# Kernel optimization log

Hardware: AMD Instinct MI355X
Metric: run time of the kernel (lower is better)

## Reference

```python
import jax, jax.numpy as jnp
import numpy as np

N_NODES = 100000


def gcn_conv(x, edge_index, W, b):
    # PyG GCNConv: add self-loops, symmetric norm, then scatter-aggregate.
    n = x.shape[0]
    x = x @ W  # [N, out]
    src = jnp.concatenate([edge_index[0], jnp.arange(n)])  # self-loops
    dst = jnp.concatenate([edge_index[1], jnp.arange(n)])
    ones = jnp.ones(src.shape[0], dtype=x.dtype)
    deg = jax.ops.segment_sum(ones, dst, num_segments=n)  # in-degree incl. self-loops
    dis = jnp.where(deg > 0, jax.lax.rsqrt(deg), 0.0)
    norm = dis[src] * dis[dst]  # [E+N]
    msg = x[src] * norm[:, None]  # gather + scale
    out = jax.ops.segment_sum(msg, dst, num_segments=n)
    return out + b


def setup_inputs() -> dict:
    key = jax.random.key(0)
    ks = jax.random.split(key, 8)
    in_dim, h1, h2, out_dim, E = 128, 128, 64, 10, 1600000
    glorot = lambda k, fi, fo: jax.random.normal(k, (fi, fo), jnp.float32) * np.sqrt(2.0 / (fi + fo))
    return {
        "x": jax.random.normal(ks[0], (N_NODES, in_dim), jnp.float32),
        "edge_index": jax.random.randint(ks[1], (2, E), 0, N_NODES, jnp.int64),
        "W1": glorot(ks[2], in_dim, h1),
        "b1": jnp.zeros((h1,), jnp.float32),
        "W2": glorot(ks[3], h1, h2),
        "b2": jnp.zeros((h2,), jnp.float32),
        "Wf": glorot(ks[4], h2, out_dim),
        "bf": jnp.zeros((out_dim,), jnp.float32),
    }


def reference(x, edge_index, W1, b1, W2, b2, Wf, bf):
    h = jax.nn.relu(gcn_conv(x, edge_index, W1, b1))
    h = jax.nn.relu(gcn_conv(h, edge_index, W2, b2))
    logits = h @ Wf + bf
    return jax.nn.softmax(logits, axis=1)
```

## Files before the change

### kernel.cpp

```cpp
#include <hip/hip_runtime.h>
#include <math.h>

#define NN 100000
#define D_IN 128
#define D_H1 128
#define D_H2 64
#define D_O 10
#define NB 256
#define BDIV 391
#define ECH 4096
#define PCAP 7168
#define S_SEG 16
#define SEGW 6250

static const size_t OFF_G1     = 0;
static const size_t OFF_G2     = 25600000;
static const size_t OFF_W1T    = 40000000;
static const size_t OFF_W2T    = 40100000;
static const size_t OFF_PART   = 76800000;
static const size_t OFF_COL    = 90000000;
static const size_t OFF_DIS    = 98000000;
static const size_t OFF_RP     = 98500000;
static const size_t OFF_RE     = 99000000;
static const size_t OFF_CUR    = 99500000;

typedef __attribute__((ext_vector_type(8))) short short8;
typedef __attribute__((ext_vector_type(4))) float floatx4;

__device__ inline unsigned int pack_bf2(float a, float b) {
  unsigned int ua = __float_as_uint(a);
  ua += 0x7fffu + ((ua >> 16) & 1u);
  unsigned int ub = __float_as_uint(b);
  ub += 0x7fffu + ((ub >> 16) & 1u);
  return (ua >> 16) | (ub & 0xffff0000u);
}
__device__ inline unsigned short bf16u(float a) {
  unsigned int ua = __float_as_uint(a);
  ua += 0x7fffu + ((ua >> 16) & 1u);
  return (unsigned short)(ua >> 16);
}
__device__ inline float bflo(unsigned int u) { return __uint_as_float(u << 16); }
__device__ inline float bfhi(unsigned int u) { return __uint_as_float(u & 0xffff0000u); }
__device__ inline short8 as_short8(uint4 u) {
  union { uint4 u4; short8 s8; } c; c.u4 = u; return c.s8;
}
__device__ inline void acc_u4(float* acc, uint4 u) {
  acc[0] += bflo(u.x); acc[1] += bfhi(u.x);
  acc[2] += bflo(u.y); acc[3] += bfhi(u.y);
  acc[4] += bflo(u.z); acc[5] += bfhi(u.z);
  acc[6] += bflo(u.w); acc[7] += bfhi(u.w);
}
__device__ inline void acc_u4s(float* acc, uint4 u, float sc) {
  acc[0] = fmaf(sc, bflo(u.x), acc[0]);
  acc[1] = fmaf(sc, bfhi(u.x), acc[1]);
  acc[2] = fmaf(sc, bflo(u.y), acc[2]);
  acc[3] = fmaf(sc, bfhi(u.y), acc[3]);
  acc[4] = fmaf(sc, bflo(u.z), acc[4]);
  acc[5] = fmaf(sc, bfhi(u.z), acc[5]);
  acc[6] = fmaf(sc, bflo(u.w), acc[6]);
  acc[7] = fmaf(sc, bfhi(u.w), acc[7]);
}

__global__ __launch_bounds__(256) void scatter_pack_kernel(
    const int* __restrict__ src, const int* __restrict__ dst,
    int* __restrict__ cursor, unsigned int* __restrict__ part,
    int E, int nchunk,
    const float* __restrict__ W1, const float* __restrict__ W2,
    unsigned short* __restrict__ w1t, unsigned short* __restrict__ w2t) {
  const int tid = threadIdx.x;
  const int bid = blockIdx.x;
  if (bid >= nchunk) {
    int pb = bid - nchunk;
    if (pb < 64) {
      int o = pb * 256 + tid;
      int nn = o >> 7, k = o & 127;
      w1t[o] = bf16u(W1[(size_t)k * D_H1 + nn]);
    } else {
      int o = (pb - 64) * 256 + tid;
      int nn = o >> 7, k = o & 127;
      w2t[o] = bf16u(W2[(size_t)k * D_H2 + nn]);
    }
    return;
  }
  __shared__ int dloc[ECH];
  __shared__ int cnt[NB];
  __shared__ int rbase[NB];
  __shared__ int rnk[NB];
  cnt[tid] = 0;
  __syncthreads();
  const int e0 = bid * ECH;
#pragma unroll
  for (int i = 0; i < ECH / 256; ++i) {
    int e = e0 + i * 256 + tid;
    int d = (e < E) ? dst[e] : -1;
    dloc[i * 256 + tid] = d;
    if (d >= 0) atomicAdd(&cnt[d / BDIV], 1);
  }
  __syncthreads();
  rbase[tid] = atomicAdd(&cursor[tid], cnt[tid]);
  rnk[tid] = 0;
  __syncthreads();
#pragma unroll
  for (int i = 0; i < ECH / 256; ++i) {
    int e = e0 + i * 256 + tid;
    if (e < E) {
      int d = dloc[i * 256 + tid];
      int s = src[e];
      int b = d / BDIV;
      int r = rbase[b] + atomicAdd(&rnk[b], 1);
      if (r < PCAP)
        part[(size_t)b * PCAP + r] =
            ((unsigned int)(d - b * BDIV) << 17) | (unsigned int)s;
    }
  }
}

#define TOT (BDIV * S_SEG)
__global__ __launch_bounds__(256) void csr_gemm_kernel(
    const unsigned int* __restrict__ part, const int* __restrict__ cursor,
    int* __restrict__ row_ptr, int* __restrict__ row_end,
    float* __restrict__ dis, int* __restrict__ col,
    const float* __restrict__ A_, const unsigned short* __restrict__ w1t,
    unsigned short* __restrict__ g1, int n) {
  __shared__ char smu[53760];
  const int tid = threadIdx.x;

  if (blockIdx.x < NB) {
    int* cnt2 = (int*)smu;
    int* col_s = (int*)(smu + 25056);
    int* wsum = (int*)(smu + 25056 + 28672);
    const int b = blockIdx.x;
    const int lo = b * BDIV;
    const int nn = min(n - lo, BDIV);
    const int ecnt = min(cursor[b], PCAP);
    const int ebase = b * PCAP;
    for (int t = tid; t <= TOT; t += 256) cnt2[t] = 0;
    __syncthreads();
    for (int i0 = 0; i0 < ecnt; i0 += 256) {
      int idx = i0 + tid;
      if (idx < ecnt) {
        unsigned int p = part[(size_t)ebase + idx];
        int s = (int)(p & 0x1FFFFu);
        atomicAdd(&cnt2[(int)(p >> 17) * S_SEG + s / SEGW], 1);
      }
    }
    __syncthreads();
    {
      const int lane = tid & 63;
      const int wv = tid >> 6;
      int carry = 0;
      for (int t0 = 0; t0 < TOT; t0 += 1024) {
        int i0 = t0 + tid * 4;
        int v0 = (i0 + 0 < TOT) ? cnt2[i0 + 0] : 0;
        int v1 = (i0 + 1 < TOT) ? cnt2[i0 + 1] : 0;
        int v2 = (i0 + 2 < TOT) ? cnt2[i0 + 2] : 0;
        int v3 = (i0 + 3 < TOT) ? cnt2[i0 + 3] : 0;
        int ts = v0 + v1 + v2 + v3;
        int incl = ts;
#pragma unroll
        for (int off = 1; off < 64; off <<= 1) {
          int o = __shfl_up(incl, off);
          if (lane >= off) incl += o;
        }
        if (lane == 63) wsum[wv] = incl;
        __syncthreads();
        int wpre = 0;
#pragma unroll
        for (int w = 0; w < 4; ++w)
          if (w < wv) wpre += wsum[w];
        int btot = wsum[0] + wsum[1] + wsum[2] + wsum[3];
        int e = carry + wpre + (incl - ts);
        __syncthreads();
        if (i0 + 0 < TOT) cnt2[i0 + 0] = e;
        if (i0 + 1 < TOT) cnt2[i0 + 1] = e + v0;
        if (i0 + 2 < TOT) cnt2[i0 + 2] = e + v0 + v1;
        if (i0 + 3 < TOT) cnt2[i0 + 3] = e + v0 + v1 + v2;
        carry += btot;
      }
      if (tid == 0) cnt2[TOT] = carry;
    }
    __syncthreads();
    for (int t = tid; t < nn; t += 256) {
      int b0 = cnt2[t * S_SEG];
      int b1 = cnt2[(t + 1) * S_SEG];
      row_ptr[lo + t] = ebase + b0;
      row_end[lo + t] = ebase + b1;
      dis[lo + t] = rsqrtf((float)(b1 - b0) + 1.0f);
    }
    __syncthreads();
    for (int i0 = 0; i0 < ecnt; i0 += 256) {
      int idx = i0 + tid;
      if (idx < ecnt) {
        unsigned int p = part[(size_t)ebase + idx];
        int s = (int)(p & 0x1FFFFu);
        int r = atomicAdd(&cnt2[(int)(p >> 17) * S_SEG + s / SEGW], 1);
        if (r < PCAP) col_s[r] = s;
      }
    }
    __syncthreads();
    for (int idx = tid; idx < ecnt; idx += 256) col[(size_t)ebase + idx] = col_s[idx];
  } else {
    constexpr int K = 128;
    constexpr int NOUT = D_H1;
    constexpr int NT = NOUT / 16;
    constexpr int LDW = K + 8;
    unsigned short* wt = (unsigned short*)smu;
    unsigned short* buf = wt;
    const int gb = blockIdx.x - NB;

    {
      const uint4* wsrc = (const uint4*)w1t;
#pragma unroll
      for (int j = 0; j < NOUT * K / (8 * 256); ++j) {
        int o = tid + j * 256;
        int row = o >> 4;
        int k8 = (o & 15) * 8;
        *(uint4*)(wt + row * LDW + k8) = wsrc[o];
      }
    }

    const int wave = tid >> 6;
    const int lane = tid & 63;
    const int quad = lane >> 4;
    const int cg = lane & 15;
    const int row0w = gb * 64 + wave * 16;

    short8 afr[4];
    {
      int row = row0w + cg;
      if (row > n - 1) row = n - 1;
#pragma unroll
      for (int kb = 0; kb < 4; ++kb) {
        const float* p = A_ + (size_t)row * K + kb * 32 + quad * 8;
        float4 v0 = *(const float4*)(p);
        float4 v1 = *(const float4*)(p + 4);
        uint4 u;
        u.x = pack_bf2(v0.x, v0.y); u.y = pack_bf2(v0.z, v0.w);
        u.z = pack_bf2(v1.x, v1.y); u.w = pack_bf2(v1.z, v1.w);
        afr[kb] = as_short8(u);
      }
    }
    __syncthreads();

    floatx4 acc[NT];
#pragma unroll
    for (int t = 0; t < NT; ++t) acc[t] = (floatx4){0.f, 0.f, 0.f, 0.f};
#pragma unroll
    for (int t = 0; t < NT; ++t) {
      const unsigned short* wrow = wt + (t * 16 + cg) * LDW;
#pragma unroll
      for (int kb = 0; kb < 4; ++kb) {
        short8 bfr = *(const short8*)(wrow + kb * 32 + quad * 8);
        acc[t] = __builtin_amdgcn_mfma_f32_16x16x32_bf16(afr[kb], bfr, acc[t], 0, 0, 0);
      }
    }
    __syncthreads();

    unsigned short* mybuf = buf + wave * 16 * LDW;
#pragma unroll
    for (int t = 0; t < NT; ++t)
#pragma unroll
      for (int r = 0; r < 4; ++r)
        mybuf[(quad * 4 + r) * LDW + t * 16 + cg] = bf16u(acc[t][r]);
    __syncthreads();

    constexpr int CHUNKS = NOUT / 8;
    constexpr int RPI = 64 / CHUNKS;
    int cid = lane % CHUNKS;
    int rs = lane / CHUNKS;
#pragma unroll
    for (int i = 0; i < 16 / RPI; ++i) {
      int r = rs + i * RPI;
      int grow = row0w + r;
      if (grow < n) {
        uint4 u = *(const uint4*)(mybuf + r * LDW + cid * 8);
        *(uint4*)(g1 + (size_t)grow * NOUT + cid * 8) = u;
      }
    }
  }
}

__global__ __launch_bounds__(256) void gather1_gemm2_kernel(
    const unsigned short* __restrict__ g, const int* __restrict__ col,
    const int* __restrict__ row_ptr, const int* __restrict__ row_end,
    const float* __restrict__ dis, const float* __restrict__ b1,
    const unsigned short* __restrict__ w2t,
    unsigned short* __restrict__ g2, int n) {
  constexpr int K = D_H1;
  constexpr int LDW = K + 8;
  constexpr int LDO = 80;
  __shared__ unsigned short wt[D_H2 * LDW];
  __shared__ unsigned short hl[16 * LDW];
  __shared__ unsigned short obuf[16 * LDO];
  const int tid = threadIdx.x;
  const int row0 = blockIdx.x * 16;

  {
    const uint4* wsrc = (const uint4*)w2t;
#pragma unroll
    for (int j = 0; j < 4; ++j) {
      int o = tid + j * 256;
      int row = o >> 4;
      int k8 = (o & 15) * 8;
      *(uint4*)(wt + row * LDW + k8) = wsrc[o];
    }
  }

  {
    const int v = row0 + (tid >> 4);
    const int c = (tid & 15) * 8;
    const int start = row_ptr[v];
    const int end = row_end[v];
    const float dv = dis[v];
    float acc[8];
#pragma unroll
    for (int q = 0; q < 8; ++q) acc[q] = 0.f;
    acc_u4s(acc, *(const uint4*)(g + (size_t)v * K + c), dv);
    int e = start;
    for (; e + 4 <= end; e += 4) {
      int s0 = col[e + 0], s1 = col[e + 1], s2 = col[e + 2], s3 = col[e + 3];
      float q0 = dis[s0], q1 = dis[s1], q2 = dis[s2], q3 = dis[s3];
      uint4 u0 = *(const uint4*)(g + (size_t)s0 * K + c);
      uint4 u1 = *(const uint4*)(g + (size_t)s1 * K + c);
      uint4 u2 = *(const uint4*)(g + (size_t)s2 * K + c);
      uint4 u3 = *(const uint4*)(g + (size_t)s3 * K + c);
      acc_u4s(acc, u0, q0); acc_u4s(acc, u1, q1);
      acc_u4s(acc, u2, q2); acc_u4s(acc, u3, q3);
    }
    for (; e < end; ++e) {
      int s = col[e];
      acc_u4s(acc, *(const uint4*)(g + (size_t)s * K + c), dis[s]);
    }
    float4 bv0 = *(const float4*)(b1 + c);
    float4 bv1 = *(const float4*)(b1 + c + 4);
    float r0 = fmaxf(dv * acc[0] + bv0.x, 0.f);
    float r1 = fmaxf(dv * acc[1] + bv0.y, 0.f);
    float r2 = fmaxf(dv * acc[2] + bv0.z, 0.f);
    float r3 = fmaxf(dv * acc[3] + bv0.w, 0.f);
    float r4 = fmaxf(dv * acc[4] + bv1.x, 0.f);
    float r5 = fmaxf(dv * acc[5] + bv1.y, 0.f);
    float r6 = fmaxf(dv * acc[6] + bv1.z, 0.f);
    float r7 = fmaxf(dv * acc[7] + bv1.w, 0.f);
    uint4 o;
    o.x = pack_bf2(r0, r1);
    o.y = pack_bf2(r2, r3);
    o.z = pack_bf2(r4, r5);
    o.w = pack_bf2(r6, r7);
    *(uint4*)(hl + (tid >> 4) * LDW + c) = o;
  }
  __syncthreads();

  {
    const int wave = tid >> 6;
    const int lane = tid & 63;
    const int quad = lane >> 4;
    const int cg = lane & 15;
    floatx4 acc = (floatx4){0.f, 0.f, 0.f, 0.f};
    const unsigned short* wrow = wt + (wave * 16 + cg) * LDW;
    const unsigned short* arow = hl + cg * LDW;
#pragma unroll
    for (int kb = 0; kb < 4; ++kb) {
      short8 afr = *(const short8*)(arow + kb * 32 + quad * 8);
      short8 bfr = *(const short8*)(wrow + kb * 32 + quad * 8);
      acc = __builtin_amdgcn_mfma_f32_16x16x32_bf16(afr, bfr, acc, 0, 0, 0);
    }
    float4 dv4 = *(const float4*)(dis + row0 + quad * 4);
    float dvs[4] = {dv4.x, dv4.y, dv4.z, dv4.w};
#pragma unroll
    for (int r = 0; r < 4; ++r)
      obuf[(quad * 4 + r) * LDO + wave * 16 + cg] = bf16u(acc[r] * dvs[r]);
  }
  __syncthreads();

  if (tid < 128) {
    int r = tid >> 3;
    int cid = tid & 7;
    uint4 u = *(const uint4*)(obuf + r * LDO + cid * 8);
    *(uint4*)(g2 + (size_t)(row0 + r) * D_H2 + cid * 8) = u;
  }
}

__global__ __launch_bounds__(256) void gather2_final_kernel(
    const unsigned short* __restrict__ g, const int* __restrict__ col,
    const int* __restrict__ row_ptr, const int* __restrict__ row_end,
    const float* __restrict__ dis, const float* __restrict__ b2,
    const float* __restrict__ Wf, const float* __restrict__ bf,
    float* __restrict__ out, int n) {
  constexpr int LDH = 72;
  __shared__ unsigned short ha[32 * LDH];
  __shared__ unsigned short wtf[16 * LDH];
  __shared__ float bfs[D_O];
  __shared__ float ls[32][12];
  const int tid = threadIdx.x;
  if (tid < 128) {
    int nn = tid >> 3;
    int k = (tid & 7) * 8;
    uint4 u;
    if (nn < D_O) {
      u.x = pack_bf2(Wf[(size_t)(k + 0) * D_O + nn], Wf[(size_t)(k + 1) * D_O + nn]);
      u.y = pack_bf2(Wf[(size_t)(k + 2) * D_O + nn], Wf[(size_t)(k + 3) * D_O + nn]);
      u.z = pack_bf2(Wf[(size_t)(k + 4) * D_O + nn], Wf[(size_t)(k + 5) * D_O + nn]);
      u.w = pack_bf2(Wf[(size_t)(k + 6) * D_O + nn], Wf[(size_t)(k + 7) * D_O + nn]);
    } else {
      u = make_uint4(0u, 0u, 0u, 0u);
    }
    *(uint4*)(wtf + nn * LDH + k) = u;
  }
  if (tid < D_O) bfs[tid] = bf[tid];

  const int gid = blockIdx.x * 256 + tid;
  const int v = gid >> 3;
  const int nl = tid >> 3;
  const int c = (tid & 7) * 8;
  if (v < n) {
    int start = row_ptr[v];
    int end = row_end[v];
    float acc[8];
#pragma unroll
    for (int q = 0; q < 8; ++q) acc[q] = 0.f;
    acc_u4(acc, *(const uint4*)(g + (size_t)v * D_H2 + c));
    int e = start;
    for (; e + 4 <= end; e += 4) {
      int s0 = col[e + 0], s1 = col[e + 1], s2 = col[e + 2], s3 = col[e + 3];
      uint4 u0 = *(const uint4*)(g + (size_t)s0 * D_H2 + c);
      uint4 u1 = *(const uint4*)(g + (size_t)s1 * D_H2 + c);
      uint4 u2 = *(const uint4*)(g + (size_t)s2 * D_H2 + c);
      uint4 u3 = *(const uint4*)(g + (size_t)s3 * D_H2 + c);
      acc_u4(acc, u0); acc_u4(acc, u1); acc_u4(acc, u2); acc_u4(acc, u3);
    }
    for (; e < end; ++e) {
      uint4 u = *(const uint4*)(g + (size_t)col[e] * D_H2 + c);
      acc_u4(acc, u);
    }
    float dv = dis[v];
    float4 bv0 = *(const float4*)(b2 + c);
    float4 bv1 = *(const float4*)(b2 + c + 4);
    float r0 = fmaxf(dv * acc[0] + bv0.x, 0.f);
    float r1 = fmaxf(dv * acc[1] + bv0.y, 0.f);
    float r2 = fmaxf(dv * acc[2] + bv0.z, 0.f);
    float r3 = fmaxf(dv * acc[3] + bv0.w, 0.f);
    float r4 = fmaxf(dv * acc[4] + bv1.x, 0.f);
    float r5 = fmaxf(dv * acc[5] + bv1.y, 0.f);
    float r6 = fmaxf(dv * acc[6] + bv1.z, 0.f);
    float r7 = fmaxf(dv * acc[7] + bv1.w, 0.f);
    uint4 o;
    o.x = pack_bf2(r0, r1);
    o.y = pack_bf2(r2, r3);
    o.z = pack_bf2(r4, r5);
    o.w = pack_bf2(r6, r7);
    *(uint4*)(ha + nl * LDH + c) = o;
  }
  __syncthreads();
  {
    const int wave = tid >> 6;
    if (wave < 2) {
      const int lane = tid & 63;
      const int quad = lane >> 4;
      const int cg = lane & 15;
      floatx4 acc = (floatx4){0.f, 0.f, 0.f, 0.f};
      const unsigned short* arow = ha + (wave * 16 + cg) * LDH;
      const unsigned short* wrow = wtf + cg * LDH;
#pragma unroll
      for (int kb = 0; kb < 2; ++kb) {
        short8 afr = *(const short8*)(arow + kb * 32 + quad * 8);
        short8 bfr = *(const short8*)(wrow + kb * 32 + quad * 8);
        acc = __builtin_amdgcn_mfma_f32_16x16x32_bf16(afr, bfr, acc, 0, 0, 0);
      }
      if (cg < D_O) {
        float bb = bfs[cg];
#pragma unroll
        for (int r = 0; r < 4; ++r)
          ls[wave * 16 + quad * 4 + r][cg] = acc[r] + bb;
      }
    }
  }
  __syncthreads();
  if (tid < 32) {
    int v2 = blockIdx.x * 32 + tid;
    if (v2 < n) {
      float m = ls[tid][0];
#pragma unroll
      for (int j = 1; j < D_O; ++j) m = fmaxf(m, ls[tid][j]);
      float s = 0.f;
      float ex[D_O];
#pragma unroll
      for (int j = 0; j < D_O; ++j) { ex[j] = expf(ls[tid][j] - m); s += ex[j]; }
      float inv = 1.0f / s;
#pragma unroll
      for (int j = 0; j < D_O; ++j) ls[tid][j] = ex[j] * inv;
    }
  }
  __syncthreads();
  for (int idx = tid; idx < 32 * D_O; idx += 256) {
    int gidx = blockIdx.x * 32 * D_O + idx;
    if (gidx < n * D_O) out[gidx] = ls[idx / D_O][idx % D_O];
  }
}

extern "C" void kernel_launch(void* const* d_in, const int* in_sizes, int n_in,
                              void* d_out, int out_size, void* d_ws, size_t ws_size,
                              hipStream_t stream) {
  const float* x  = (const float*)d_in[0];
  const int*   ei = (const int*)d_in[1];
  const float* W1 = (const float*)d_in[2];
  const float* b1 = (const float*)d_in[3];
  const float* W2 = (const float*)d_in[4];
  const float* b2 = (const float*)d_in[5];
  const float* Wf = (const float*)d_in[6];
  const float* bf = (const float*)d_in[7];
  float* out = (float*)d_out;

  const int E = in_sizes[1] / 2;
  const int* src = ei;
  const int* dst = ei + E;

  char* ws = (char*)d_ws;
  unsigned short* g1 = (unsigned short*)(ws + OFF_G1);
  unsigned short* g2 = (unsigned short*)(ws + OFF_G2);
  unsigned short* w1t = (unsigned short*)(ws + OFF_W1T);
  unsigned short* w2t = (unsigned short*)(ws + OFF_W2T);
  unsigned int* part = (unsigned int*)(ws + OFF_PART);
  int*   col     = (int*)(ws + OFF_COL);
  float* dis     = (float*)(ws + OFF_DIS);
  int*   row_ptr = (int*)(ws + OFF_RP);
  int*   row_end = (int*)(ws + OFF_RE);
  int*   cursor  = (int*)(ws + OFF_CUR);

  const int nchunk = (E + ECH - 1) / ECH;

  hipMemsetAsync(cursor, 0, NB * sizeof(int), stream);

  scatter_pack_kernel<<<nchunk + 96, 256, 0, stream>>>(
      src, dst, cursor, part, E, nchunk, W1, W2, w1t, w2t);

  csr_gemm_kernel<<<NB + (NN + 63) / 64, 256, 0, stream>>>(
      part, cursor, row_ptr, row_end, dis, col, x, w1t, g1, NN);

  gather1_gemm2_kernel<<<NN / 16, 256, 0, stream>>>(
      g1, col, row_ptr, row_end, dis, b1, w2t, g2, NN);

  gather2_final_kernel<<<(NN + 31) / 32, 256, 0, stream>>>(
      g2, col, row_ptr, row_end, dis, b2, Wf, bf, out, NN);
}
```

Measured before the change: 240.5 us.

## Split feature matrices into column planes and gather each plane separately

Stores the layer features in column-plane layouts (16-wide planes for layer 1, 8-wide for layer 2) so each gather block reads only a narrow slice per node. The intent is better cache locality for random neighbour gathers, since each plane is small enough to stay resident in cache. The source-side normalisation moves into the GEMM epilogue. The CSR build drops the source-segment sort, and the fused kernels are split into separate csr, gemm1, gather1, gemm2, gather2 and head kernels. This adds launches and extra round trips through memory for the intermediate activations, and neighbour lists are no longer sorted by source.

```diff
diff --git a/kernel.cpp b/kernel.cpp
--- a/kernel.cpp
+++ b/kernel.cpp
@@ -10,19 +10,19 @@
 #define BDIV 391
 #define ECH 4096
 #define PCAP 7168
-#define S_SEG 16
-#define SEGW 6250
-
-static const size_t OFF_G1     = 0;
-static const size_t OFF_G2     = 25600000;
-static const size_t OFF_W1T    = 40000000;
-static const size_t OFF_W2T    = 40100000;
-static const size_t OFF_PART   = 76800000;
-static const size_t OFF_COL    = 90000000;
-static const size_t OFF_DIS    = 98000000;
-static const size_t OFF_RP     = 98500000;
-static const size_t OFF_RE     = 99000000;
-static const size_t OFF_CUR    = 99500000;
+
+
+static const size_t OFF_G1  = 0;
+static const size_t OFF_H   = 25600000;
+static const size_t OFF_G2  = 51200000;
+static const size_t OFF_H2  = 64000000;
+static const size_t OFF_W2T = 76800000;
+static const size_t OFF_PART= 76900000;
+static const size_t OFF_COL = 84300000;
+static const size_t OFF_DIS = 91700000;
+static const size_t OFF_RP  = 92200000;
+static const size_t OFF_RE  = 92600000;
+static const size_t OFF_CUR = 93000000;
 
 typedef __attribute__((ext_vector_type(8))) short short8;
 typedef __attribute__((ext_vector_type(4))) float floatx4;
@@ -50,36 +50,18 @@
   acc[4] += bflo(u.z); acc[5] += bfhi(u.z);
   acc[6] += bflo(u.w); acc[7] += bfhi(u.w);
 }
-__device__ inline void acc_u4s(float* acc, uint4 u, float sc) {
-  acc[0] = fmaf(sc, bflo(u.x), acc[0]);
-  acc[1] = fmaf(sc, bfhi(u.x), acc[1]);
-  acc[2] = fmaf(sc, bflo(u.y), acc[2]);
-  acc[3] = fmaf(sc, bfhi(u.y), acc[3]);
-  acc[4] = fmaf(sc, bflo(u.z), acc[4]);
-  acc[5] = fmaf(sc, bfhi(u.z), acc[5]);
-  acc[6] = fmaf(sc, bflo(u.w), acc[6]);
-  acc[7] = fmaf(sc, bfhi(u.w), acc[7]);
-}
 
 __global__ __launch_bounds__(256) void scatter_pack_kernel(
     const int* __restrict__ src, const int* __restrict__ dst,
     int* __restrict__ cursor, unsigned int* __restrict__ part,
     int E, int nchunk,
-    const float* __restrict__ W1, const float* __restrict__ W2,
-    unsigned short* __restrict__ w1t, unsigned short* __restrict__ w2t) {
+    const float* __restrict__ W2, unsigned short* __restrict__ w2t) {
   const int tid = threadIdx.x;
   const int bid = blockIdx.x;
   if (bid >= nchunk) {
-    int pb = bid - nchunk;
-    if (pb < 64) {
-      int o = pb * 256 + tid;
-      int nn = o >> 7, k = o & 127;
-      w1t[o] = bf16u(W1[(size_t)k * D_H1 + nn]);
-    } else {
-      int o = (pb - 64) * 256 + tid;
-      int nn = o >> 7, k = o & 127;
-      w2t[o] = bf16u(W2[(size_t)k * D_H2 + nn]);
-    }
+    int o = (bid - nchunk) * 256 + tid;
+    int nn = o >> 7, k = o & 127;
+    w2t[o] = bf16u(W2[(size_t)k * D_H2 + nn]);
     return;
   }
   __shared__ int dloc[ECH];
@@ -115,185 +97,214 @@
   }
 }
 
-#define TOT (BDIV * S_SEG)
-__global__ __launch_bounds__(256) void csr_gemm_kernel(
+__global__ __launch_bounds__(256) void csr_kernel(
     const unsigned int* __restrict__ part, const int* __restrict__ cursor,
     int* __restrict__ row_ptr, int* __restrict__ row_end,
-    float* __restrict__ dis, int* __restrict__ col,
-    const float* __restrict__ A_, const unsigned short* __restrict__ w1t,
-    unsigned short* __restrict__ g1, int n) {
-  __shared__ char smu[53760];
-  const int tid = threadIdx.x;
-
-  if (blockIdx.x < NB) {
-    int* cnt2 = (int*)smu;
-    int* col_s = (int*)(smu + 25056);
-    int* wsum = (int*)(smu + 25056 + 28672);
-    const int b = blockIdx.x;
-    const int lo = b * BDIV;
-    const int nn = min(n - lo, BDIV);
-    const int ecnt = min(cursor[b], PCAP);
-    const int ebase = b * PCAP;
-    for (int t = tid; t <= TOT; t += 256) cnt2[t] = 0;
+    float* __restrict__ dis, int* __restrict__ col, int n) {
+  __shared__ int sm[256];
+  __shared__ int ldeg[BDIV + 1];
+  __shared__ int lofs[BDIV + 1];
+  __shared__ int col_s[PCAP];
+  const int tid = threadIdx.x;
+  const int b = blockIdx.x;
+  const int lo = b * BDIV;
+  const int nn = min(n - lo, BDIV);
+  const int ecnt = min(cursor[b], PCAP);
+  const int ebase = b * PCAP;
+  for (int t = tid; t <= BDIV; t += 256) ldeg[t] = 0;
+  __syncthreads();
+  for (int i0 = 0; i0 < ecnt; i0 += 256) {
+    int idx = i0 + tid;
+    if (idx < ecnt) atomicAdd(&ldeg[part[(size_t)ebase + idx] >> 17], 1);
+  }
+  __syncthreads();
+  int carry = 0;
+  for (int t0 = 0; t0 < BDIV + 1; t0 += 256) {
+    int idx = t0 + tid;
+    int v = (idx <= BDIV) ? ldeg[idx] : 0;
+    sm[tid] = v;
     __syncthreads();
-    for (int i0 = 0; i0 < ecnt; i0 += 256) {
-      int idx = i0 + tid;
-      if (idx < ecnt) {
-        unsigned int p = part[(size_t)ebase + idx];
-        int s = (int)(p & 0x1FFFFu);
-        atomicAdd(&cnt2[(int)(p >> 17) * S_SEG + s / SEGW], 1);
-      }
-    }
+#pragma unroll
+    for (int off = 1; off < 256; off <<= 1) {
+      int t2 = (tid >= off) ? sm[tid - off] : 0;
+      __syncthreads();
+      sm[tid] += t2;
+      __syncthreads();
+    }
+    int incl = sm[tid];
+    int ttot = sm[255];
     __syncthreads();
-    {
-      const int lane = tid & 63;
-      const int wv = tid >> 6;
-      int carry = 0;
-      for (int t0 = 0; t0 < TOT; t0 += 1024) {
-        int i0 = t0 + tid * 4;
-        int v0 = (i0 + 0 < TOT) ? cnt2[i0 + 0] : 0;
-        int v1 = (i0 + 1 < TOT) ? cnt2[i0 + 1] : 0;
-        int v2 = (i0 + 2 < TOT) ? cnt2[i0 + 2] : 0;
-        int v3 = (i0 + 3 < TOT) ? cnt2[i0 + 3] : 0;
-        int ts = v0 + v1 + v2 + v3;
-        int incl = ts;
-#pragma unroll
-        for (int off = 1; off < 64; off <<= 1) {
-          int o = __shfl_up(incl, off);
-          if (lane >= off) incl += o;
-        }
-        if (lane == 63) wsum[wv] = incl;
-        __syncthreads();
-        int wpre = 0;
-#pragma unroll
-        for (int w = 0; w < 4; ++w)
-          if (w < wv) wpre += wsum[w];
-        int btot = wsum[0] + wsum[1] + wsum[2] + wsum[3];
-        int e = carry + wpre + (incl - ts);
-        __syncthreads();
-        if (i0 + 0 < TOT) cnt2[i0 + 0] = e;
-        if (i0 + 1 < TOT) cnt2[i0 + 1] = e + v0;
-        if (i0 + 2 < TOT) cnt2[i0 + 2] = e + v0 + v1;
-        if (i0 + 3 < TOT) cnt2[i0 + 3] = e + v0 + v1 + v2;
-        carry += btot;
-      }
-      if (tid == 0) cnt2[TOT] = carry;
-    }
-    __syncthreads();
-    for (int t = tid; t < nn; t += 256) {
-      int b0 = cnt2[t * S_SEG];
-      int b1 = cnt2[(t + 1) * S_SEG];
-      row_ptr[lo + t] = ebase + b0;
-      row_end[lo + t] = ebase + b1;
-      dis[lo + t] = rsqrtf((float)(b1 - b0) + 1.0f);
-    }
-    __syncthreads();
-    for (int i0 = 0; i0 < ecnt; i0 += 256) {
-      int idx = i0 + tid;
-      if (idx < ecnt) {
-        unsigned int p = part[(size_t)ebase + idx];
-        int s = (int)(p & 0x1FFFFu);
-        int r = atomicAdd(&cnt2[(int)(p >> 17) * S_SEG + s / SEGW], 1);
-        if (r < PCAP) col_s[r] = s;
-      }
-    }
-    __syncthreads();
-    for (int idx = tid; idx < ecnt; idx += 256) col[(size_t)ebase + idx] = col_s[idx];
-  } else {
-    constexpr int K = 128;
-    constexpr int NOUT = D_H1;
-    constexpr int NT = NOUT / 16;
-    constexpr int LDW = K + 8;
-    unsigned short* wt = (unsigned short*)smu;
-    unsigned short* buf = wt;
-    const int gb = blockIdx.x - NB;
-
-    {
-      const uint4* wsrc = (const uint4*)w1t;
-#pragma unroll
-      for (int j = 0; j < NOUT * K / (8 * 256); ++j) {
-        int o = tid + j * 256;
-        int row = o >> 4;
-        int k8 = (o & 15) * 8;
-        *(uint4*)(wt + row * LDW + k8) = wsrc[o];
-      }
-    }
-
-    const int wave = tid >> 6;
-    const int lane = tid & 63;
-    const int quad = lane >> 4;
-    const int cg = lane & 15;
-    const int row0w = gb * 64 + wave * 16;
-
-    short8 afr[4];
-    {
-      int row = row0w + cg;
-      if (row > n - 1) row = n - 1;
-#pragma unroll
-      for (int kb = 0; kb < 4; ++kb) {
-        const float* p = A_ + (size_t)row * K + kb * 32 + quad * 8;
-        float4 v0 = *(const float4*)(p);
-        float4 v1 = *(const float4*)(p + 4);
-        uint4 u;
-        u.x = pack_bf2(v0.x, v0.y); u.y = pack_bf2(v0.z, v0.w);
-        u.z = pack_bf2(v1.x, v1.y); u.w = pack_bf2(v1.z, v1.w);
-        afr[kb] = as_short8(u);
-      }
-    }
-    __syncthreads();
-
-    floatx4 acc[NT];
-#pragma unroll
-    for (int t = 0; t < NT; ++t) acc[t] = (floatx4){0.f, 0.f, 0.f, 0.f};
-#pragma unroll
-    for (int t = 0; t < NT; ++t) {
-      const unsigned short* wrow = wt + (t * 16 + cg) * LDW;
-#pragma unroll
-      for (int kb = 0; kb < 4; ++kb) {
-        short8 bfr = *(const short8*)(wrow + kb * 32 + quad * 8);
-        acc[t] = __builtin_amdgcn_mfma_f32_16x16x32_bf16(afr[kb], bfr, acc[t], 0, 0, 0);
-      }
-    }
-    __syncthreads();
-
-    unsigned short* mybuf = buf + wave * 16 * LDW;
-#pragma unroll
-    for (int t = 0; t < NT; ++t)
-#pragma unroll
-      for (int r = 0; r < 4; ++r)
-        mybuf[(quad * 4 + r) * LDW + t * 16 + cg] = bf16u(acc[t][r]);
-    __syncthreads();
-
-    constexpr int CHUNKS = NOUT / 8;
-    constexpr int RPI = 64 / CHUNKS;
-    int cid = lane % CHUNKS;
-    int rs = lane / CHUNKS;
-#pragma unroll
-    for (int i = 0; i < 16 / RPI; ++i) {
-      int r = rs + i * RPI;
-      int grow = row0w + r;
-      if (grow < n) {
-        uint4 u = *(const uint4*)(mybuf + r * LDW + cid * 8);
-        *(uint4*)(g1 + (size_t)grow * NOUT + cid * 8) = u;
-      }
-    }
-  }
-}
-
-__global__ __launch_bounds__(256) void gather1_gemm2_kernel(
-    const unsigned short* __restrict__ g, const int* __restrict__ col,
+    if (idx <= BDIV) lofs[idx] = carry + incl - v;
+    carry += ttot;
+  }
+  __syncthreads();
+  for (int t = tid; t < nn; t += 256) {
+    int d = ldeg[t];
+    row_ptr[lo + t] = ebase + lofs[t];
+    row_end[lo + t] = ebase + lofs[t] + d;
+    dis[lo + t] = rsqrtf((float)d + 1.0f);
+  }
+  __syncthreads();
+  for (int i0 = 0; i0 < ecnt; i0 += 256) {
+    int idx = i0 + tid;
+    if (idx < ecnt) {
+      unsigned int p = part[(size_t)ebase + idx];
+      int r = atomicAdd(&lofs[p >> 17], 1);
+      col_s[r] = (int)(p & 0x1FFFFu);
+    }
+  }
+  __syncthreads();
+  for (int idx = tid; idx < ecnt; idx += 256) col[(size_t)ebase + idx] = col_s[idx];
+}
+
+__global__ __launch_bounds__(256) void gemm1_kernel(
+    const float* __restrict__ A_, const float* __restrict__ W1,
+    const float* __restrict__ dis, unsigned short* __restrict__ g1p, int n) {
+  constexpr int K = 128;
+  constexpr int NOUT = D_H1;
+  constexpr int NT = NOUT / 16;
+  constexpr int LDW = K + 8;
+  __shared__ unsigned short wt[NOUT * LDW];
+  unsigned short* buf = wt;
+  const int tid = threadIdx.x;
+
+  {
+    int nn = tid & 127;
+    int k0 = (tid >> 7) * 64;
+#pragma unroll
+    for (int kb = 0; kb < 8; ++kb) {
+      int k = k0 + kb * 8;
+      unsigned int u0 = pack_bf2(W1[(size_t)(k + 0) * NOUT + nn], W1[(size_t)(k + 1) * NOUT + nn]);
+      unsigned int u1 = pack_bf2(W1[(size_t)(k + 2) * NOUT + nn], W1[(size_t)(k + 3) * NOUT + nn]);
+      unsigned int u2 = pack_bf2(W1[(size_t)(k + 4) * NOUT + nn], W1[(size_t)(k + 5) * NOUT + nn]);
+      unsigned int u3 = pack_bf2(W1[(size_t)(k + 6) * NOUT + nn], W1[(size_t)(k + 7) * NOUT + nn]);
+      *(uint4*)(wt + nn * LDW + k) = make_uint4(u0, u1, u2, u3);
+    }
+  }
+
+  const int wave = tid >> 6;
+  const int lane = tid & 63;
+  const int quad = lane >> 4;
+  const int cg = lane & 15;
+  const int row0blk = blockIdx.x * 64;
+  const int row0w = row0blk + wave * 16;
+
+  short8 afr[4];
+  {
+    int row = row0w + cg;
+    if (row > n - 1) row = n - 1;
+#pragma unroll
+    for (int kb = 0; kb < 4; ++kb) {
+      const float* p = A_ + (size_t)row * K + kb * 32 + quad * 8;
+      float4 v0 = *(const float4*)(p);
+      float4 v1 = *(const float4*)(p + 4);
+      uint4 u;
+      u.x = pack_bf2(v0.x, v0.y); u.y = pack_bf2(v0.z, v0.w);
+      u.z = pack_bf2(v1.x, v1.y); u.w = pack_bf2(v1.z, v1.w);
+      afr[kb] = as_short8(u);
+    }
+  }
+  __syncthreads();
+
+  floatx4 acc[NT];
+#pragma unroll
+  for (int t = 0; t < NT; ++t) acc[t] = (floatx4){0.f, 0.f, 0.f, 0.f};
+#pragma unroll
+  for (int t = 0; t < NT; ++t) {
+    const unsigned short* wrow = wt + (t * 16 + cg) * LDW;
+#pragma unroll
+    for (int kb = 0; kb < 4; ++kb) {
+      short8 bfr = *(const short8*)(wrow + kb * 32 + quad * 8);
+      acc[t] = __builtin_amdgcn_mfma_f32_16x16x32_bf16(afr[kb], bfr, acc[t], 0, 0, 0);
+    }
+  }
+  __syncthreads();
+
+  float4 dv4 = *(const float4*)(dis + row0w + quad * 4);
+  float dvs[4] = {dv4.x, dv4.y, dv4.z, dv4.w};
+  unsigned short* mybuf = buf + wave * 16 * LDW;
+#pragma unroll
+  for (int t = 0; t < NT; ++t)
+#pragma unroll
+    for (int r = 0; r < 4; ++r)
+      mybuf[(quad * 4 + r) * LDW + t * 16 + cg] = bf16u(acc[t][r] * dvs[r]);
+  __syncthreads();
+
+#pragma unroll
+  for (int it = 0; it < 4; ++it) {
+    int idx = it * 256 + tid;
+    int half = idx & 1;
+    int row = (idx >> 1) & 63;
+    int plane = idx >> 7;
+    int grow = row0blk + row;
+    if (grow < n) {
+      uint4 u = *(const uint4*)(buf + row * LDW + plane * 16 + half * 8);
+      *(uint4*)(g1p + (size_t)plane * NN * 16 + (size_t)grow * 16 + half * 8) = u;
+    }
+  }
+}
+
+__global__ __launch_bounds__(256) void gather1_kernel(
+    const unsigned short* __restrict__ g1p, const int* __restrict__ col,
     const int* __restrict__ row_ptr, const int* __restrict__ row_end,
     const float* __restrict__ dis, const float* __restrict__ b1,
-    const unsigned short* __restrict__ w2t,
-    unsigned short* __restrict__ g2, int n) {
-  constexpr int K = D_H1;
+    unsigned short* __restrict__ hp, int n) {
+  const int tid = threadIdx.x;
+  const int p = blockIdx.x & 7;
+  const int v = (blockIdx.x >> 3) * 128 + (tid >> 1);
+  const int half = tid & 1;
+  if (v >= n) return;
+  const unsigned short* gp = g1p + (size_t)p * NN * 16;
+  const int start = row_ptr[v];
+  const int end = row_end[v];
+  float acc[8];
+#pragma unroll
+  for (int q = 0; q < 8; ++q) acc[q] = 0.f;
+  acc_u4(acc, *(const uint4*)(gp + (size_t)v * 16 + half * 8));
+  int e = start;
+  for (; e + 4 <= end; e += 4) {
+    int s0 = col[e + 0], s1 = col[e + 1], s2 = col[e + 2], s3 = col[e + 3];
+    uint4 u0 = *(const uint4*)(gp + (size_t)s0 * 16 + half * 8);
+    uint4 u1 = *(const uint4*)(gp + (size_t)s1 * 16 + half * 8);
+    uint4 u2 = *(const uint4*)(gp + (size_t)s2 * 16 + half * 8);
+    uint4 u3 = *(const uint4*)(gp + (size_t)s3 * 16 + half * 8);
+    acc_u4(acc, u0); acc_u4(acc, u1); acc_u4(acc, u2); acc_u4(acc, u3);
+  }
+  for (; e < end; ++e) {
+    uint4 u = *(const uint4*)(gp + (size_t)col[e] * 16 + half * 8);
+    acc_u4(acc, u);
+  }
+  const float dv = dis[v];
+  const float* bp = b1 + p * 16 + half * 8;
+  float4 bv0 = *(const float4*)(bp);
+  float4 bv1 = *(const float4*)(bp + 4);
+  float r0 = fmaxf(dv * acc[0] + bv0.x, 0.f);
+  float r1 = fmaxf(dv * acc[1] + bv0.y, 0.f);
+  float r2 = fmaxf(dv * acc[2] + bv0.z, 0.f);
+  float r3 = fmaxf(dv * acc[3] + bv0.w, 0.f);
+  float r4 = fmaxf(dv * acc[4] + bv1.x, 0.f);
+  float r5 = fmaxf(dv * acc[5] + bv1.y, 0.f);
+  float r6 = fmaxf(dv * acc[6] + bv1.z, 0.f);
+  float r7 = fmaxf(dv * acc[7] + bv1.w, 0.f);
+  uint4 o;
+  o.x = pack_bf2(r0, r1);
+  o.y = pack_bf2(r2, r3);
+  o.z = pack_bf2(r4, r5);
+  o.w = pack_bf2(r6, r7);
+  *(uint4*)(hp + (size_t)p * NN * 16 + (size_t)v * 16 + half * 8) = o;
+}
+
+__global__ __launch_bounds__(256) void gemm2_kernel(
+    const unsigned short* __restrict__ hp, const unsigned short* __restrict__ w2t,
+    const float* __restrict__ dis, unsigned short* __restrict__ g2p, int n) {
+  constexpr int K = 128;
+  constexpr int NOUT = D_H2;
+  constexpr int NT = NOUT / 16;
   constexpr int LDW = K + 8;
-  constexpr int LDO = 80;
-  __shared__ unsigned short wt[D_H2 * LDW];
-  __shared__ unsigned short hl[16 * LDW];
-  __shared__ unsigned short obuf[16 * LDO];
-  const int tid = threadIdx.x;
-  const int row0 = blockIdx.x * 16;
+  constexpr int LDB = 72;
+  __shared__ unsigned short wt[NOUT * LDW];
+  __shared__ unsigned short buf[64 * LDB];
+  const int tid = threadIdx.x;
 
   {
     const uint4* wsrc = (const uint4*)w2t;
@@ -306,86 +317,115 @@
     }
   }
 
+  const int wave = tid >> 6;
+  const int lane = tid & 63;
+  const int quad = lane >> 4;
+  const int cg = lane & 15;
+  const int row0blk = blockIdx.x * 64;
+  const int row0w = row0blk + wave * 16;
+
+  short8 afr[4];
   {
-    const int v = row0 + (tid >> 4);
-    const int c = (tid & 15) * 8;
-    const int start = row_ptr[v];
-    const int end = row_end[v];
-    const float dv = dis[v];
-    float acc[8];
-#pragma unroll
-    for (int q = 0; q < 8; ++q) acc[q] = 0.f;
-    acc_u4s(acc, *(const uint4*)(g + (size_t)v * K + c), dv);
-    int e = start;
-    for (; e + 4 <= end; e += 4) {
-      int s0 = col[e + 0], s1 = col[e + 1], s2 = col[e + 2], s3 = col[e + 3];
-      float q0 = dis[s0], q1 = dis[s1], q2 = dis[s2], q3 = dis[s3];
-      uint4 u0 = *(const uint4*)(g + (size_t)s0 * K + c);
-      uint4 u1 = *(const uint4*)(g + (size_t)s1 * K + c);
-      uint4 u2 = *(const uint4*)(g + (size_t)s2 * K + c);
-      uint4 u3 = *(const uint4*)(g + (size_t)s3 * K + c);
-      acc_u4s(acc, u0, q0); acc_u4s(acc, u1, q1);
-      acc_u4s(acc, u2, q2); acc_u4s(acc, u3, q3);
-    }
-    for (; e < end; ++e) {
-      int s = col[e];
-      acc_u4s(acc, *(const uint4*)(g + (size_t)s * K + c), dis[s]);
-    }
-    float4 bv0 = *(const float4*)(b1 + c);
-    float4 bv1 = *(const float4*)(b1 + c + 4);
-    float r0 = fmaxf(dv * acc[0] + bv0.x, 0.f);
-    float r1 = fmaxf(dv * acc[1] + bv0.y, 0.f);
-    float r2 = fmaxf(dv * acc[2] + bv0.z, 0.f);
-    float r3 = fmaxf(dv * acc[3] + bv0.w, 0.f);
-    float r4 = fmaxf(dv * acc[4] + bv1.x, 0.f);
-    float r5 = fmaxf(dv * acc[5] + bv1.y, 0.f);
-    float r6 = fmaxf(dv * acc[6] + bv1.z, 0.f);
-    float r7 = fmaxf(dv * acc[7] + bv1.w, 0.f);
-    uint4 o;
-    o.x = pack_bf2(r0, r1);
-    o.y = pack_bf2(r2, r3);
-    o.z = pack_bf2(r4, r5);
-    o.w = pack_bf2(r6, r7);
-    *(uint4*)(hl + (tid >> 4) * LDW + c) = o;
-  }
-  __syncthreads();
-
-  {
-    const int wave = tid >> 6;
-    const int lane = tid & 63;
-    const int quad = lane >> 4;
-    const int cg = lane & 15;
-    floatx4 acc = (floatx4){0.f, 0.f, 0.f, 0.f};
-    const unsigned short* wrow = wt + (wave * 16 + cg) * LDW;
-    const unsigned short* arow = hl + cg * LDW;
+    int row = row0w + cg;
+    if (row > n - 1) row = n - 1;
 #pragma unroll
     for (int kb = 0; kb < 4; ++kb) {
-      short8 afr = *(const short8*)(arow + kb * 32 + quad * 8);
+      int plane = kb * 2 + (quad >> 1);
+      const unsigned short* pa =
+          hp + (size_t)plane * NN * 16 + (size_t)row * 16 + (quad & 1) * 8;
+      afr[kb] = *(const short8*)(pa);
+    }
+  }
+  __syncthreads();
+
+  floatx4 acc[NT];
+#pragma unroll
+  for (int t = 0; t < NT; ++t) acc[t] = (floatx4){0.f, 0.f, 0.f, 0.f};
+#pragma unroll
+  for (int t = 0; t < NT; ++t) {
+    const unsigned short* wrow = wt + (t * 16 + cg) * LDW;
+#pragma unroll
+    for (int kb = 0; kb < 4; ++kb) {
       short8 bfr = *(const short8*)(wrow + kb * 32 + quad * 8);
-      acc = __builtin_amdgcn_mfma_f32_16x16x32_bf16(afr, bfr, acc, 0, 0, 0);
-    }
-    float4 dv4 = *(const float4*)(dis + row0 + quad * 4);
-    float dvs[4] = {dv4.x, dv4.y, dv4.z, dv4.w};
+      acc[t] = __builtin_amdgcn_mfma_f32_16x16x32_bf16(afr[kb], bfr, acc[t], 0, 0, 0);
+    }
+  }
+
+  float4 dv4 = *(const float4*)(dis + row0w + quad * 4);
+  float dvs[4] = {dv4.x, dv4.y, dv4.z, dv4.w};
+  unsigned short* mybuf = buf + wave * 16 * LDB;
+#pragma unroll
+  for (int t = 0; t < NT; ++t)
 #pragma unroll
     for (int r = 0; r < 4; ++r)
-      obuf[(quad * 4 + r) * LDO + wave * 16 + cg] = bf16u(acc[r] * dvs[r]);
-  }
-  __syncthreads();
-
-  if (tid < 128) {
-    int r = tid >> 3;
-    int cid = tid & 7;
-    uint4 u = *(const uint4*)(obuf + r * LDO + cid * 8);
-    *(uint4*)(g2 + (size_t)(row0 + r) * D_H2 + cid * 8) = u;
-  }
-}
-
-__global__ __launch_bounds__(256) void gather2_final_kernel(
-    const unsigned short* __restrict__ g, const int* __restrict__ col,
+      mybuf[(quad * 4 + r) * LDB + t * 16 + cg] = bf16u(acc[t][r] * dvs[r]);
+  __syncthreads();
+
+#pragma unroll
+  for (int it = 0; it < 2; ++it) {
+    int idx = it * 256 + tid;
+    int row = idx & 63;
+    int c = idx >> 6;
+    int grow = row0blk + row;
+    if (grow < n) {
+      uint4 u = *(const uint4*)(buf + row * LDB + c * 8);
+      *(uint4*)(g2p + (size_t)c * NN * 8 + (size_t)grow * 8) = u;
+    }
+  }
+}
+
+__global__ __launch_bounds__(256) void gather2_kernel(
+    const unsigned short* __restrict__ g2p, const int* __restrict__ col,
     const int* __restrict__ row_ptr, const int* __restrict__ row_end,
     const float* __restrict__ dis, const float* __restrict__ b2,
-    const float* __restrict__ Wf, const float* __restrict__ bf,
-    float* __restrict__ out, int n) {
+    unsigned short* __restrict__ h2p, int n) {
+  const int tid = threadIdx.x;
+  const int p = blockIdx.x & 7;
+  const int v = (blockIdx.x >> 3) * 256 + tid;
+  if (v >= n) return;
+  const unsigned short* gp = g2p + (size_t)p * NN * 8;
+  const int start = row_ptr[v];
+  const int end = row_end[v];
+  float acc[8];
+#pragma unroll
+  for (int q = 0; q < 8; ++q) acc[q] = 0.f;
+  acc_u4(acc, *(const uint4*)(gp + (size_t)v * 8));
+  int e = start;
+  for (; e + 4 <= end; e += 4) {
+    int s0 = col[e + 0], s1 = col[e + 1], s2 = col[e + 2], s3 = col[e + 3];
+    uint4 u0 = *(const uint4*)(gp + (size_t)s0 * 8);
+    uint4 u1 = *(const uint4*)(gp + (size_t)s1 * 8);
+    uint4 u2 = *(const uint4*)(gp + (size_t)s2 * 8);
+    uint4 u3 = *(const uint4*)(gp + (size_t)s3 * 8);
+    acc_u4(acc, u0); acc_u4(acc, u1); acc_u4(acc, u2); acc_u4(acc, u3);
+  }
+  for (; e < end; ++e) {
+    uint4 u = *(const uint4*)(gp + (size_t)col[e] * 8);
+    acc_u4(acc, u);
+  }
+  const float dv = dis[v];
+  const float* bp = b2 + p * 8;
+  float4 bv0 = *(const float4*)(bp);
+  float4 bv1 = *(const float4*)(bp + 4);
+  float r0 = fmaxf(dv * acc[0] + bv0.x, 0.f);
+  float r1 = fmaxf(dv * acc[1] + bv0.y, 0.f);
+  float r2 = fmaxf(dv * acc[2] + bv0.z, 0.f);
+  float r3 = fmaxf(dv * acc[3] + bv0.w, 0.f);
+  float r4 = fmaxf(dv * acc[4] + bv1.x, 0.f);
+  float r5 = fmaxf(dv * acc[5] + bv1.y, 0.f);
+  float r6 = fmaxf(dv * acc[6] + bv1.z, 0.f);
+  float r7 = fmaxf(dv * acc[7] + bv1.w, 0.f);
+  uint4 o;
+  o.x = pack_bf2(r0, r1);
+  o.y = pack_bf2(r2, r3);
+  o.z = pack_bf2(r4, r5);
+  o.w = pack_bf2(r6, r7);
+  *(uint4*)(h2p + (size_t)p * NN * 8 + (size_t)v * 8) = o;
+}
+
+__global__ __launch_bounds__(256) void head_kernel(
+    const unsigned short* __restrict__ h2p, const float* __restrict__ Wf,
+    const float* __restrict__ bf, float* __restrict__ out, int n) {
   constexpr int LDH = 72;
   __shared__ unsigned short ha[32 * LDH];
   __shared__ unsigned short wtf[16 * LDH];
@@ -408,47 +448,12 @@
   }
   if (tid < D_O) bfs[tid] = bf[tid];
 
-  const int gid = blockIdx.x * 256 + tid;
-  const int v = gid >> 3;
   const int nl = tid >> 3;
-  const int c = (tid & 7) * 8;
+  const int pl = tid & 7;
+  const int v = blockIdx.x * 32 + nl;
   if (v < n) {
-    int start = row_ptr[v];
-    int end = row_end[v];
-    float acc[8];
-#pragma unroll
-    for (int q = 0; q < 8; ++q) acc[q] = 0.f;
-    acc_u4(acc, *(const uint4*)(g + (size_t)v * D_H2 + c));
-    int e = start;
-    for (; e + 4 <= end; e += 4) {
-      int s0 = col[e + 0], s1 = col[e + 1], s2 = col[e + 2], s3 = col[e + 3];
-      uint4 u0 = *(const uint4*)(g + (size_t)s0 * D_H2 + c);
-      uint4 u1 = *(const uint4*)(g + (size_t)s1 * D_H2 + c);
-      uint4 u2 = *(const uint4*)(g + (size_t)s2 * D_H2 + c);
-      uint4 u3 = *(const uint4*)(g + (size_t)s3 * D_H2 + c);
-      acc_u4(acc, u0); acc_u4(acc, u1); acc_u4(acc, u2); acc_u4(acc, u3);
-    }
-    for (; e < end; ++e) {
-      uint4 u = *(const uint4*)(g + (size_t)col[e] * D_H2 + c);
-      acc_u4(acc, u);
-    }
-    float dv = dis[v];
-    float4 bv0 = *(const float4*)(b2 + c);
-    float4 bv1 = *(const float4*)(b2 + c + 4);
-    float r0 = fmaxf(dv * acc[0] + bv0.x, 0.f);
-    float r1 = fmaxf(dv * acc[1] + bv0.y, 0.f);
-    float r2 = fmaxf(dv * acc[2] + bv0.z, 0.f);
-    float r3 = fmaxf(dv * acc[3] + bv0.w, 0.f);
-    float r4 = fmaxf(dv * acc[4] + bv1.x, 0.f);
-    float r5 = fmaxf(dv * acc[5] + bv1.y, 0.f);
-    float r6 = fmaxf(dv * acc[6] + bv1.z, 0.f);
-    float r7 = fmaxf(dv * acc[7] + bv1.w, 0.f);
-    uint4 o;
-    o.x = pack_bf2(r0, r1);
-    o.y = pack_bf2(r2, r3);
-    o.z = pack_bf2(r4, r5);
-    o.w = pack_bf2(r6, r7);
-    *(uint4*)(ha + nl * LDH + c) = o;
+    uint4 u = *(const uint4*)(h2p + (size_t)pl * NN * 8 + (size_t)v * 8);
+    *(uint4*)(ha + nl * LDH + pl * 8) = u;
   }
   __syncthreads();
   {
@@ -515,9 +520,10 @@
   const int* dst = ei + E;
 
   char* ws = (char*)d_ws;
-  unsigned short* g1 = (unsigned short*)(ws + OFF_G1);
-  unsigned short* g2 = (unsigned short*)(ws + OFF_G2);
-  unsigned short* w1t = (unsigned short*)(ws + OFF_W1T);
+  unsigned short* g1p = (unsigned short*)(ws + OFF_G1);
+  unsigned short* hp  = (unsigned short*)(ws + OFF_H);
+  unsigned short* g2p = (unsigned short*)(ws + OFF_G2);
+  unsigned short* h2p = (unsigned short*)(ws + OFF_H2);
   unsigned short* w2t = (unsigned short*)(ws + OFF_W2T);
   unsigned int* part = (unsigned int*)(ws + OFF_PART);
   int*   col     = (int*)(ws + OFF_COL);
@@ -530,15 +536,20 @@
 
   hipMemsetAsync(cursor, 0, NB * sizeof(int), stream);
 
-  scatter_pack_kernel<<<nchunk + 96, 256, 0, stream>>>(
-      src, dst, cursor, part, E, nchunk, W1, W2, w1t, w2t);
-
-  csr_gemm_kernel<<<NB + (NN + 63) / 64, 256, 0, stream>>>(
-      part, cursor, row_ptr, row_end, dis, col, x, w1t, g1, NN);
-
-  gather1_gemm2_kernel<<<NN / 16, 256, 0, stream>>>(
-      g1, col, row_ptr, row_end, dis, b1, w2t, g2, NN);
-
-  gather2_final_kernel<<<(NN + 31) / 32, 256, 0, stream>>>(
-      g2, col, row_ptr, row_end, dis, b2, Wf, bf, out, NN);
-}
+  scatter_pack_kernel<<<nchunk + 32, 256, 0, stream>>>(
+      src, dst, cursor, part, E, nchunk, W2, w2t);
+
+  csr_kernel<<<NB, 256, 0, stream>>>(part, cursor, row_ptr, row_end, dis, col, NN);
+
+  gemm1_kernel<<<(NN + 63) / 64, 256, 0, stream>>>(x, W1, dis, g1p, NN);
+
+  gather1_kernel<<<((NN + 127) / 128) * 8, 256, 0, stream>>>(
+      g1p, col, row_ptr, row_end, dis, b1, hp, NN);
+
+  gemm2_kernel<<<(NN + 63) / 64, 256, 0, stream>>>(hp, w2t, dis, g2p, NN);
+
+  gather2_kernel<<<((NN + 255) / 256) * 8, 256, 0, stream>>>(
+      g2p, col, row_ptr, row_end, dis, b2, h2p, NN);
+
+  head_kernel<<<(NN + 31) / 32, 256, 0, stream>>>(h2p, Wf, bf, out, NN);
+}
```

New measurement: 323.7 us. 34.6% more time.
